# Kernel optimization log

Hardware: AMD Instinct MI355X
Metric: run time of the kernel (lower is better)

Reference implementation:

```python
import jax, jax.numpy as jnp
import numpy as np
from jax import lax

# dims: hidden D, heads H, key head dim DK, value head dim DV (=DK*expand_v), conv size K
B, T, D = 2, 1024, 1024
H, DK, DV, K = 8, 128, 256, 4
EPS = 1e-5  # RMSNorm eps


def short_conv(x, w):
    # depthwise causal conv1d + silu (FLA ShortConvolution, bias=False, activation='silu')
    # x: [B,T,C], w: [C,K]
    Kc = w.shape[-1]
    xp = jnp.pad(x, ((0, 0), (Kc - 1, 0), (0, 0))).transpose(0, 2, 1)  # [B,C,T+K-1]
    y = lax.conv_general_dilated(xp, w[:, None, :], (1,), 'VALID',
                                 feature_group_count=w.shape[0])  # [B,C,T]
    return jax.nn.silu(y.transpose(0, 2, 1))


def l2norm(x):
    return x * lax.rsqrt(jnp.sum(x * x, axis=-1, keepdims=True) + 1e-6)


def gated_delta_rule(q, k, v, g, beta):
    # q,k: [B,T,H,DK]; v: [B,T,H,DV]; g,beta: [B,T,H]
    # recurrence: S_t = exp(g_t)*S_{t-1}; u_t = beta_t*(v_t - k_t^T S_t); S_t += k_t u_t^T; o_t = q_t^T S_t
    scale = q.shape[-1] ** -0.5
    q = l2norm(q) * scale
    k = l2norm(k)
    qT, kT, vT = (a.transpose(1, 0, 2, 3) for a in (q, k, v))  # time-major
    gT, bT = g.transpose(1, 0, 2), beta.transpose(1, 0, 2)
    S0 = jnp.zeros((q.shape[0], q.shape[2], q.shape[3], v.shape[3]), q.dtype)  # [B,H,DK,DV]

    def step(S, inp):
        q_t, k_t, v_t, g_t, b_t = inp
        S = S * jnp.exp(g_t)[..., None, None]
        u = (v_t - jnp.einsum('bhk,bhkv->bhv', k_t, S)) * b_t[..., None]
        S = S + jnp.einsum('bhk,bhv->bhkv', k_t, u)
        o_t = jnp.einsum('bhk,bhkv->bhv', q_t, S)
        return S, o_t

    _, oT = lax.scan(step, S0, (qT, kT, vT, gT, bT))
    return oT.transpose(1, 0, 2, 3)  # [B,T,H,DV]


def setup_inputs() -> dict:
    key = jax.random.key(0)
    ks = jax.random.split(key, 16)
    s = 0.02
    dt = jax.random.uniform(ks[10], (H,), minval=1e-3, maxval=0.1)
    return {
        'x': jax.random.normal(ks[0], (B, T, D), jnp.float32),
        'Wq': jax.random.normal(ks[1], (D, H * DK), jnp.float32) * s,
        'Wk': jax.random.normal(ks[2], (D, H * DK), jnp.float32) * s,
        'Wv': jax.random.normal(ks[3], (D, H * DV), jnp.float32) * s,
        'conv_q': jax.random.normal(ks[4], (H * DK, K), jnp.float32) * 0.2,
        'conv_k': jax.random.normal(ks[5], (H * DK, K), jnp.float32) * 0.2,
        'conv_v': jax.random.normal(ks[6], (H * DV, K), jnp.float32) * 0.2,
        'Wb': jax.random.normal(ks[7], (D, H), jnp.float32) * s,
        'Wa': jax.random.normal(ks[8], (D, H), jnp.float32) * s,
        'A_log': jnp.log(jax.random.uniform(ks[9], (H,), minval=1.0, maxval=16.0)),
        'dt_bias': jnp.log(jnp.expm1(dt)),
        'Wg': jax.random.normal(ks[11], (D, H * DV), jnp.float32) * s,
        'norm_w': jnp.ones((DV,), jnp.float32),
        'Wo': jax.random.normal(ks[12], (H * DV, D), jnp.float32) * s,
    }


def reference(x, Wq, Wk, Wv, conv_q, conv_k, conv_v, Wb, Wa, A_log, dt_bias, Wg, norm_w, Wo):
    Bx, Tx = x.shape[0], x.shape[1]
    q = short_conv(x @ Wq, conv_q).reshape(Bx, Tx, H, DK)
    k = short_conv(x @ Wk, conv_k).reshape(Bx, Tx, H, DK)
    v = short_conv(x @ Wv, conv_v).reshape(Bx, Tx, H, DV)
    beta = jax.nn.sigmoid(x @ Wb)                                  # [B,T,H]
    g = -jnp.exp(A_log) * jax.nn.softplus(x @ Wa + dt_bias)       # [B,T,H], log-decay <= 0
    o = gated_delta_rule(q, k, v, g, beta)                         # [B,T,H,DV]
    # fused gated RMSNorm: rmsnorm(o)*w * silu(g_proj)
    gv = (x @ Wg).reshape(Bx, Tx, H, DV)
    o = o * lax.rsqrt(jnp.mean(o * o, axis=-1, keepdims=True) + EPS) * norm_w
    o = o * jax.nn.silu(gv)
    return o.reshape(Bx, Tx, H * DV) @ Wo
```

## Files before the change

### kernel.cpp

```cpp
#include <hip/hip_runtime.h>
#include <hip/hip_bf16.h>
#include <math.h>

constexpr int Bc = 2, Tc = 1024, Dc = 1024, Hc = 8, DKc = 128, DVc = 256;
constexpr int BT_ROWS = Bc * Tc;
constexpr float QSCALE = 0.08838834764831845f;
constexpr int NCHUNK = 16, CHUNK = 64;

constexpr size_t OF_XB   = 0;
constexpr size_t OF_KBAR = 1048576;
constexpr size_t OF_BTG  = 3145728;
constexpr size_t OF_QPRE = 4194304;
constexpr size_t OF_KPRE = 6291456;
constexpr size_t OF_VPRE = 8388608;
constexpr size_t OF_Q    = 12582912;
constexpr size_t OF_K    = 14680064;
constexpr size_t OF_V    = 4194304;
constexpr size_t OF_G    = 16777216;
constexpr size_t OF_BETA = 16793600;
constexpr size_t OF_O    = 8388608;
constexpr size_t OF_GV   = 12582912;
constexpr size_t OF_OOB  = 4194304;
constexpr size_t OF_WQT  = 12582912;
constexpr size_t OF_WKT  = 13107200;
constexpr size_t OF_WVT  = 13631488;
constexpr size_t OF_WGT  = 1048576;
constexpr size_t OF_WOT  = 2097152;

using short8 = __attribute__((ext_vector_type(8))) short;
using short4v = __attribute__((ext_vector_type(4))) short;
using f32x4  = __attribute__((ext_vector_type(4))) float;

__device__ inline unsigned short f2bf(float f) {
  unsigned int u = __builtin_bit_cast(unsigned int, f);
  u += 0x7FFFu + ((u >> 16) & 1u);
  return (unsigned short)(u >> 16);
}

__device__ inline void gload16(const void* g, void* l) {
  __builtin_amdgcn_global_load_lds(
      (const __attribute__((address_space(1))) unsigned int*)g,
      (__attribute__((address_space(3))) unsigned int*)l, 16, 0, 0);
}

__global__ __launch_bounds__(256) void cvt_bf16(const float* __restrict__ X,
                                                unsigned short* __restrict__ Y) {
  int i = (blockIdx.x * 256 + threadIdx.x) * 4;
  float4 f = *(const float4*)&X[i];
  short4v o = {(short)f2bf(f.x), (short)f2bf(f.y), (short)f2bf(f.z), (short)f2bf(f.w)};
  *(short4v*)&Y[i] = o;
}

__global__ __launch_bounds__(256) void transposeW(const float* __restrict__ W,
                                                  unsigned short* __restrict__ WT,
                                                  int K, int N) {
  __shared__ unsigned short Ls[64 * 66];
  const int n0 = blockIdx.x * 64, k0 = blockIdx.y * 64;
  const int t = threadIdx.x;
  {
    int r = t >> 2, c0 = (t & 3) * 16;
    const float* src = &W[(size_t)(k0 + r) * N + n0 + c0];
#pragma unroll
    for (int m = 0; m < 4; ++m) {
      float4 f = *(const float4*)&src[m * 4];
      unsigned short* p = &Ls[r * 66 + c0 + m * 4];
      p[0] = f2bf(f.x); p[1] = f2bf(f.y); p[2] = f2bf(f.z); p[3] = f2bf(f.w);
    }
  }
  __syncthreads();
  {
    int n = t >> 2, k4 = (t & 3) * 16;
    short8 o0, o1;
#pragma unroll
    for (int j = 0; j < 8; ++j) {
      o0[j] = (short)Ls[(k4 + j) * 66 + n];
      o1[j] = (short)Ls[(k4 + 8 + j) * 66 + n];
    }
    unsigned short* dst = &WT[(size_t)(n0 + n) * K + k0 + k4];
    *(short8*)dst = o0;
    *(short8*)(dst + 8) = o1;
  }
}

template <int TN>
__global__ __launch_bounds__(256) void gemm_nt(const unsigned short* __restrict__ A,
                                               const unsigned short* __restrict__ BT,
                                               float* __restrict__ C,
                                               int M, int N, int K) {
  constexpr int NF = TN / 32;
  __shared__ unsigned short As[128 * 64];
  __shared__ unsigned short Bs[TN * 64];
  const int tid = threadIdx.x, l = tid & 63, w = tid >> 6;
  const int m0 = blockIdx.y * 128, n0 = blockIdx.x * TN;
  const int wm = (w >> 1) * 64, wn = (w & 1) * (TN / 2);
  const int fr = l & 15, hk = l >> 4;
  const int srow = l >> 3, swin = l & 7;
  f32x4 acc[4][NF] = {};

  for (int k0 = 0; k0 < K; k0 += 64) {
#pragma unroll
    for (int i = 0; i < 4; ++i) {
      int ch = i * 4 + w;
      int row = ch * 8 + srow;
      gload16((const char*)(A + (size_t)(m0 + row) * K + k0) + ((swin ^ (row & 7)) * 16),
              (char*)As + ch * 1024);
    }
#pragma unroll
    for (int i = 0; i < TN / 32; ++i) {
      int ch = i * 4 + w;
      int row = ch * 8 + srow;
      gload16((const char*)(BT + (size_t)(n0 + row) * K + k0) + ((swin ^ (row & 7)) * 16),
              (char*)Bs + ch * 1024);
    }
    __syncthreads();
#pragma unroll
    for (int ks = 0; ks < 2; ++ks) {
      short8 a[4], b[NF];
#pragma unroll
      for (int mf = 0; mf < 4; ++mf) {
        int row = wm + mf * 16 + fr;
        a[mf] = *(const short8*)((const char*)As + row * 128 + (((hk + 4 * ks) ^ (row & 7)) * 16));
      }
#pragma unroll
      for (int nf = 0; nf < NF; ++nf) {
        int row = wn + nf * 16 + fr;
        b[nf] = *(const short8*)((const char*)Bs + row * 128 + (((hk + 4 * ks) ^ (row & 7)) * 16));
      }
#pragma unroll
      for (int mf = 0; mf < 4; ++mf)
#pragma unroll
        for (int nf = 0; nf < NF; ++nf)
          acc[mf][nf] = __builtin_amdgcn_mfma_f32_16x16x32_bf16(a[mf], b[nf], acc[mf][nf], 0, 0, 0);
    }
    __syncthreads();
  }
  const int orow = (l >> 4) * 4;
#pragma unroll
  for (int mf = 0; mf < 4; ++mf)
#pragma unroll
    for (int nf = 0; nf < NF; ++nf)
#pragma unroll
      for (int r = 0; r < 4; ++r)
        C[(size_t)(m0 + wm + mf * 16 + orow + r) * N + n0 + wn + nf * 16 + fr] = acc[mf][nf][r];
}

__global__ __launch_bounds__(256) void conv_silu(const float* __restrict__ X,
                                                 const float* __restrict__ W,
                                                 float* __restrict__ Y, int C) {
  int c = blockIdx.x * 256 + threadIdx.x;
  if (c >= C) return;
  int b  = blockIdx.z;
  int t0 = blockIdx.y * 32;
  float4 w = *(const float4*)&W[c * 4];
  const float* xp = X + (size_t)b * Tc * C + c;
  float* yp = Y + (size_t)b * Tc * C + c;
  float x0 = (t0 >= 3) ? xp[(size_t)(t0 - 3) * C] : 0.f;
  float x1 = (t0 >= 2) ? xp[(size_t)(t0 - 2) * C] : 0.f;
  float x2 = (t0 >= 1) ? xp[(size_t)(t0 - 1) * C] : 0.f;
  for (int t = t0; t < t0 + 32; ++t) {
    float x3 = xp[(size_t)t * C];
    float a  = w.x * x0 + w.y * x1 + w.z * x2 + w.w * x3;
    float y  = a / (1.f + __expf(-a));
    yp[(size_t)t * C] = y;
    x0 = x1; x1 = x2; x2 = x3;
  }
}

__global__ __launch_bounds__(256) void beta_g_kernel(const float* __restrict__ X,
                                                     const float* __restrict__ Wb,
                                                     const float* __restrict__ Wa,
                                                     const float* __restrict__ A_log,
                                                     const float* __restrict__ dt_bias,
                                                     float* __restrict__ beta,
                                                     float* __restrict__ glog) {
  int w    = blockIdx.x * 4 + (threadIdx.x >> 6);
  int lane = threadIdx.x & 63;
  int h  = w & 7;
  int bt = w >> 3;
  const float* x = X + (size_t)bt * Dc;
  float sb = 0.f, sa = 0.f;
#pragma unroll
  for (int i = 0; i < 16; ++i) {
    int d = lane + 64 * i;
    float xv = x[d];
    sb = fmaf(xv, Wb[d * 8 + h], sb);
    sa = fmaf(xv, Wa[d * 8 + h], sa);
  }
#pragma unroll
  for (int m = 1; m < 64; m <<= 1) {
    sb += __shfl_xor(sb, m);
    sa += __shfl_xor(sa, m);
  }
  if (lane == 0) {
    beta[w] = 1.f / (1.f + expf(-sb));
    float z  = sa + dt_bias[h];
    float sp = (z > 20.f) ? z : log1pf(expf(z));
    glog[w]  = -expf(A_log[h]) * sp;
  }
}

__global__ __launch_bounds__(256) void l2norm_qk(float* __restrict__ Q, float* __restrict__ K) {
  int w    = blockIdx.x * 4 + (threadIdx.x >> 6);
  int lane = threadIdx.x & 63;
  int h = w & 7;
  size_t bt = (size_t)(w >> 3);
  float* qp = Q + bt * (Hc * DKc) + h * DKc + lane * 2;
  float* kp = K + bt * (Hc * DKc) + h * DKc + lane * 2;
  float2 q2 = *(float2*)qp;
  float2 k2 = *(float2*)kp;
  float sq = q2.x * q2.x + q2.y * q2.y;
  float sk = k2.x * k2.x + k2.y * k2.y;
#pragma unroll
  for (int m = 1; m < 64; m <<= 1) {
    sq += __shfl_xor(sq, m);
    sk += __shfl_xor(sk, m);
  }
  float rq = rsqrtf(sq + 1e-6f) * QSCALE;
  float rk = rsqrtf(sk + 1e-6f);
  q2.x *= rq; q2.y *= rq;
  k2.x *= rk; k2.y *= rk;
  *(float2*)qp = q2;
  *(float2*)kp = k2;
}

__global__ __launch_bounds__(256) void phase1(const float* __restrict__ Q,
                                              const float* __restrict__ K,
                                              float* __restrict__ V,
                                              const float* __restrict__ G,
                                              const float* __restrict__ BETA,
                                              float* __restrict__ Kbar,
                                              float* __restrict__ BTm) {
  constexpr int SK = 68;
  __shared__ float sm[25984];
  float* kcT  = sm;
  float* qcT  = sm + 8704;
  float* vld  = sm;
  float* Amat = sm + 17408;
  float* Mmat = sm + 21568;
  float* cs   = sm + 25728;
  float* bet  = sm + 25856;
  float* wk   = sm + 25920;
  const int tid = threadIdx.x;
  const int c = blockIdx.x, bh = blockIdx.y;
  const int b = bh >> 3, h = bh & 7;
  const int t0 = c * CHUNK;
  const size_t cb = (size_t)bh * NCHUNK + c;

  if (tid < 64) {
    cs[tid]  = G[((size_t)(b * Tc + t0 + tid)) * 8 + h];
    bet[tid] = BETA[((size_t)(b * Tc + t0 + tid)) * 8 + h];
  }
  {
    int r = tid >> 2, dq = (tid & 3) * 32;
    const float4* kg = (const float4*)&K[((size_t)(b * Tc + t0 + r)) * 1024 + h * 128 + dq];
    const float4* qg = (const float4*)&Q[((size_t)(b * Tc + t0 + r)) * 1024 + h * 128 + dq];
#pragma unroll
    for (int m = 0; m < 8; ++m) {
      float4 kv = kg[m], qv = qg[m];
      int d = dq + m * 4;
      kcT[(d + 0) * SK + r] = kv.x; kcT[(d + 1) * SK + r] = kv.y;
      kcT[(d + 2) * SK + r] = kv.z; kcT[(d + 3) * SK + r] = kv.w;
      qcT[(d + 0) * SK + r] = qv.x; qcT[(d + 1) * SK + r] = qv.y;
      qcT[(d + 2) * SK + r] = qv.z; qcT[(d + 3) * SK + r] = qv.w;
    }
  }
  __syncthreads();
  if (tid == 0) {
    float a = 0.f;
    for (int i = 0; i < 64; ++i) { a += cs[i]; cs[i] = a; }
  }
  __syncthreads();
  if (tid < 64) {
    float gv_ = __expf(cs[tid]);
    wk[tid]  = bet[tid] * gv_;
  }
  for (int e = tid; e < 4096; e += 256) {
    int i = e >> 6, s = e & 63;
    float av = 0.f;
    if (s < i) {
      float acc = 0.f;
      for (int d = 0; d < 128; ++d) acc += kcT[d * SK + i] * kcT[d * SK + s];
      av = bet[i] * __expf(cs[i] - cs[s]) * acc;
    }
    Amat[i * 65 + s] = av;
  }
  for (int e = tid; e < 4096; e += 256) {
    int s = e >> 6, i = e & 63;
    float outv = 0.f;
    if (s <= i) {
      float acc = 0.f;
      for (int d = 0; d < 128; ++d) acc += qcT[d * SK + i] * kcT[d * SK + s];
      outv = __expf(cs[i] - cs[s]) * acc;
    }
    BTm[cb * 4096 + (size_t)s * 64 + i] = outv;
  }
  __syncthreads();
  if (tid < 64) {
    int j = tid;
    for (int i = 0; i < 64; ++i) {
      float m = (i == j) ? 1.f : 0.f;
      for (int s = 0; s < i; ++s) m -= Amat[i * 65 + s] * Mmat[s * 65 + j];
      Mmat[i * 65 + j] = m;
    }
  }
  __syncthreads();
  for (int e = tid; e < 2048; e += 256) {
    int i = e & 63, d0 = ((e >> 6) & 31) * 4;
    float a0 = 0, a1 = 0, a2 = 0, a3 = 0;
#pragma unroll 4
    for (int s = 0; s < 64; ++s) {
      float m_ = Mmat[i * 65 + s] * wk[s];
      a0 = fmaf(m_, kcT[(d0 + 0) * SK + s], a0);
      a1 = fmaf(m_, kcT[(d0 + 1) * SK + s], a1);
      a2 = fmaf(m_, kcT[(d0 + 2) * SK + s], a2);
      a3 = fmaf(m_, kcT[(d0 + 3) * SK + s], a3);
    }
    float4 w4 = {a0, a1, a2, a3};
    *(float4*)&Kbar[cb * 8192 + (size_t)i * 128 + d0] = w4;
  }
  __syncthreads();
  {
    int r = tid >> 2, j0 = (tid & 3) * 64;
    const float4* vg = (const float4*)&V[((size_t)(b * Tc + t0 + r)) * 2048 + h * 256 + j0];
#pragma unroll
    for (int m = 0; m < 16; ++m) *(float4*)&vld[r * 256 + j0 + m * 4] = vg[m];
  }
  __syncthreads();
  for (int e = tid; e < 4096; e += 256) {
    int i = e >> 6, j0 = (e & 63) * 4;
    float a0 = 0, a1 = 0, a2 = 0, a3 = 0;
    for (int s = 0; s < 64; ++s) {
      float m_ = Mmat[i * 65 + s] * bet[s];
      float4 vv = *(const float4*)&vld[s * 256 + j0];
      a0 = fmaf(m_, vv.x, a0); a1 = fmaf(m_, vv.y, a1);
      a2 = fmaf(m_, vv.z, a2); a3 = fmaf(m_, vv.w, a3);
    }
    float4 o4 = {a0, a1, a2, a3};
    *(float4*)&V[((size_t)(b * Tc + t0 + i)) * 2048 + h * 256 + j0] = o4;
  }
}

__global__ __launch_bounds__(256) void phase2(const float* __restrict__ KbarG,
                                              const float* __restrict__ BTmG,
                                              const float* __restrict__ GL,
                                              const float* __restrict__ Qp,
                                              const float* __restrict__ Kp,
                                              const float* __restrict__ VBAR,
                                              float* __restrict__ O) {
  __shared__ float S[16 * 132];
  __shared__ float KbL[64 * 128];
  __shared__ float qcL[64 * 128];
  __shared__ float K2L[64 * 128];
  __shared__ float BcL[64 * 64];
  __shared__ float uL[64 * 20];
  __shared__ float csL[64], rsL[64], gamL[64];
  const int tid = threadIdx.x;
  const int l = tid & 63, w = tid >> 6;
  const int jb = blockIdx.y, bh = blockIdx.x;
  const int b = bh >> 3, h = bh & 7;
  const int i = l;
  const int j0 = w * 4;
  const int swzi = (i & 7) << 2;
  const int d0u = (tid & 31) * 4;
  const int jq = tid >> 5;
  const size_t colbase = (size_t)h * 256 + jb * 16;

  for (int e = tid; e < 16 * 132; e += 256) S[e] = 0.f;

  for (int c = 0; c < NCHUNK; ++c) {
    const size_t cb = (size_t)bh * NCHUNK + c;
    const int bT0 = b * Tc + c * CHUNK;
    __syncthreads();
    if (tid < 64) {
      float gi = GL[((size_t)(bT0 + tid)) * 8 + h];
#pragma unroll
      for (int off = 1; off < 64; off <<= 1) {
        float p = __shfl_up(gi, off);
        if (tid >= off) gi += p;
      }
      csL[tid] = gi;
    }
    {
      const char* kbg = (const char*)(KbarG + cb * 8192);
#pragma unroll
      for (int ic = 0; ic < 8; ++ic) {
        int ch = ic * 4 + w;
        int row = 2 * ch + (l >> 5);
        int inrow = (l & 31) * 16;
        int swz = inrow ^ ((row & 7) << 4);
        gload16(kbg + row * 512 + swz, (char*)KbL + ch * 1024);
        gload16((const char*)(Qp + ((size_t)(bT0 + row)) * 1024 + h * 128) + swz,
                (char*)qcL + ch * 1024);
        gload16((const char*)(Kp + ((size_t)(bT0 + row)) * 1024 + h * 128) + inrow,
                (char*)K2L + ch * 1024);
      }
      const char* btg = (const char*)(BTmG + cb * 4096);
#pragma unroll
      for (int ic = 0; ic < 4; ++ic) {
        int ch = ic * 4 + w;
        gload16(btg + ch * 1024 + l * 16, (char*)BcL + ch * 1024);
      }
    }
    __syncthreads();
    if (tid < 64) {
      gamL[tid] = __expf(csL[tid]);
      rsL[tid]  = __expf(csL[63] - csL[tid]);
    }
    float ua[4] = {}, ra[4] = {};
#pragma unroll 4
    for (int d = 0; d < 128; d += 4) {
      int ds = d ^ swzi;
      float4 kb = *(const float4*)&KbL[i * 128 + ds];
      float4 qg = *(const float4*)&qcL[i * 128 + ds];
#pragma unroll
      for (int jj = 0; jj < 4; ++jj) {
        float4 s4 = *(const float4*)&S[(j0 + jj) * 132 + d];
        ua[jj] = fmaf(kb.x, s4.x, fmaf(kb.y, s4.y, fmaf(kb.z, s4.z, fmaf(kb.w, s4.w, ua[jj]))));
        ra[jj] = fmaf(qg.x, s4.x, fmaf(qg.y, s4.y, fmaf(qg.z, s4.z, fmaf(qg.w, s4.w, ra[jj]))));
      }
    }
    float4 vb = *(const float4*)&VBAR[((size_t)(bT0 + i)) * 2048 + colbase + j0];
    float4 uf = {vb.x - ua[0], vb.y - ua[1], vb.z - ua[2], vb.w - ua[3]};
    *(float4*)&uL[i * 20 + j0] = uf;
    __syncthreads();
    float ba[4] = {};
#pragma unroll 4
    for (int s = 0; s < 64; ++s) {
      float bv = BcL[s * 64 + i];
      float4 u4 = *(const float4*)&uL[s * 20 + j0];
      ba[0] = fmaf(bv, u4.x, ba[0]); ba[1] = fmaf(bv, u4.y, ba[1]);
      ba[2] = fmaf(bv, u4.z, ba[2]); ba[3] = fmaf(bv, u4.w, ba[3]);
    }
    float gi = gamL[i];
    float4 o4 = {gi * ra[0] + ba[0], gi * ra[1] + ba[1],
                 gi * ra[2] + ba[2], gi * ra[3] + ba[3]};
    *(float4*)&O[((size_t)(bT0 + i)) * 2048 + colbase + j0] = o4;
    float sa[2][4] = {};
#pragma unroll 4
    for (int s = 0; s < 64; ++s) {
      float4 k2 = *(const float4*)&K2L[s * 128 + d0u];
      float rv = rsL[s];
      float u0 = uL[s * 20 + 2 * jq] * rv;
      float u1 = uL[s * 20 + 2 * jq + 1] * rv;
      sa[0][0] = fmaf(k2.x, u0, sa[0][0]); sa[0][1] = fmaf(k2.y, u0, sa[0][1]);
      sa[0][2] = fmaf(k2.z, u0, sa[0][2]); sa[0][3] = fmaf(k2.w, u0, sa[0][3]);
      sa[1][0] = fmaf(k2.x, u1, sa[1][0]); sa[1][1] = fmaf(k2.y, u1, sa[1][1]);
      sa[1][2] = fmaf(k2.z, u1, sa[1][2]); sa[1][3] = fmaf(k2.w, u1, sa[1][3]);
    }
    float gC = gamL[63];
#pragma unroll
    for (int jj = 0; jj < 2; ++jj) {
      float4 sv = *(const float4*)&S[(2 * jq + jj) * 132 + d0u];
      sv.x = fmaf(gC, sv.x, sa[jj][0]); sv.y = fmaf(gC, sv.y, sa[jj][1]);
      sv.z = fmaf(gC, sv.z, sa[jj][2]); sv.w = fmaf(gC, sv.w, sa[jj][3]);
      *(float4*)&S[(2 * jq + jj) * 132 + d0u] = sv;
    }
  }
}

__global__ __launch_bounds__(256) void gated_rmsnorm(const float* __restrict__ O,
                                                     const float* __restrict__ GV,
                                                     const float* __restrict__ NW,
                                                     unsigned short* __restrict__ OO) {
  int w    = blockIdx.x * 4 + (threadIdx.x >> 6);
  int lane = threadIdx.x & 63;
  size_t base = (size_t)w * DVc;
  float4 o4 = *(const float4*)&O[base + lane * 4];
  float ss = o4.x * o4.x + o4.y * o4.y + o4.z * o4.z + o4.w * o4.w;
#pragma unroll
  for (int m = 1; m < 64; m <<= 1) ss += __shfl_xor(ss, m);
  float r = rsqrtf(ss * (1.f / 256.f) + 1e-5f);
  float4 g4 = *(const float4*)&GV[base + lane * 4];
  float4 w4 = *(const float4*)&NW[lane * 4];
  float4 out;
  out.x = o4.x * r * w4.x * (g4.x / (1.f + __expf(-g4.x)));
  out.y = o4.y * r * w4.y * (g4.y / (1.f + __expf(-g4.y)));
  out.z = o4.z * r * w4.z * (g4.z / (1.f + __expf(-g4.z)));
  out.w = o4.w * r * w4.w * (g4.w / (1.f + __expf(-g4.w)));
  short4v ob = {(short)f2bf(out.x), (short)f2bf(out.y), (short)f2bf(out.z), (short)f2bf(out.w)};
  *(short4v*)&OO[base + lane * 4] = ob;
}

extern "C" void kernel_launch(void* const* d_in, const int* in_sizes, int n_in,
                              void* d_out, int out_size, void* d_ws, size_t ws_size,
                              hipStream_t stream) {
  const float* x       = (const float*)d_in[0];
  const float* Wq      = (const float*)d_in[1];
  const float* Wk      = (const float*)d_in[2];
  const float* Wv      = (const float*)d_in[3];
  const float* conv_q  = (const float*)d_in[4];
  const float* conv_k  = (const float*)d_in[5];
  const float* conv_v  = (const float*)d_in[6];
  const float* Wb      = (const float*)d_in[7];
  const float* Wa      = (const float*)d_in[8];
  const float* A_log   = (const float*)d_in[9];
  const float* dt_bias = (const float*)d_in[10];
  const float* Wg      = (const float*)d_in[11];
  const float* norm_w  = (const float*)d_in[12];
  const float* Wo      = (const float*)d_in[13];
  float* out = (float*)d_out;
  float* ws  = (float*)d_ws;

  unsigned short* xb  = (unsigned short*)(ws + OF_XB);
  unsigned short* WqT = (unsigned short*)(ws + OF_WQT);
  unsigned short* WkT = (unsigned short*)(ws + OF_WKT);
  unsigned short* WvT = (unsigned short*)(ws + OF_WVT);
  unsigned short* WgT = (unsigned short*)(ws + OF_WGT);
  unsigned short* WoT = (unsigned short*)(ws + OF_WOT);
  unsigned short* oob = (unsigned short*)(ws + OF_OOB);
  float* qpre  = ws + OF_QPRE;
  float* kpre  = ws + OF_KPRE;
  float* vpre  = ws + OF_VPRE;
  float* q     = ws + OF_Q;
  float* k     = ws + OF_K;
  float* v     = ws + OF_V;
  float* glog  = ws + OF_G;
  float* beta  = ws + OF_BETA;
  float* Kbar  = ws + OF_KBAR;
  float* BTm   = ws + OF_BTG;
  float* o     = ws + OF_O;
  float* gv    = ws + OF_GV;

  dim3 blk(256);

  cvt_bf16<<<dim3(2048), blk, 0, stream>>>(x, xb);
  transposeW<<<dim3(16, 16), blk, 0, stream>>>(Wq, WqT, 1024, 1024);
  transposeW<<<dim3(16, 16), blk, 0, stream>>>(Wk, WkT, 1024, 1024);
  transposeW<<<dim3(32, 16), blk, 0, stream>>>(Wv, WvT, 1024, 2048);

  gemm_nt<64><<<dim3(16, 16), blk, 0, stream>>>(xb, WqT, qpre, BT_ROWS, 1024, 1024);
  gemm_nt<64><<<dim3(16, 16), blk, 0, stream>>>(xb, WkT, kpre, BT_ROWS, 1024, 1024);
  gemm_nt<128><<<dim3(16, 16), blk, 0, stream>>>(xb, WvT, vpre, BT_ROWS, 2048, 1024);

  beta_g_kernel<<<dim3(BT_ROWS * Hc / 4), blk, 0, stream>>>(x, Wb, Wa, A_log, dt_bias, beta, glog);

  conv_silu<<<dim3(1024 / 256, Tc / 32, Bc), blk, 0, stream>>>(qpre, conv_q, q, 1024);
  conv_silu<<<dim3(1024 / 256, Tc / 32, Bc), blk, 0, stream>>>(kpre, conv_k, k, 1024);
  conv_silu<<<dim3(2048 / 256, Tc / 32, Bc), blk, 0, stream>>>(vpre, conv_v, v, 2048);

  l2norm_qk<<<dim3(BT_ROWS * Hc / 4), blk, 0, stream>>>(q, k);

  phase1<<<dim3(NCHUNK, Bc * Hc), blk, 0, stream>>>(q, k, v, glog, beta, Kbar, BTm);
  phase2<<<dim3(Bc * Hc, 16), blk, 0, stream>>>(Kbar, BTm, glog, q, k, v, o);

  transposeW<<<dim3(32, 16), blk, 0, stream>>>(Wg, WgT, 1024, 2048);
  gemm_nt<128><<<dim3(16, 16), blk, 0, stream>>>(xb, WgT, gv, BT_ROWS, 2048, 1024);

  transposeW<<<dim3(16, 32), blk, 0, stream>>>(Wo, WoT, 2048, 1024);
  gated_rmsnorm<<<dim3(BT_ROWS * Hc / 4), blk, 0, stream>>>(o, gv, norm_w, oob);

  gemm_nt<64><<<dim3(16, 16), blk, 0, stream>>>(oob, WoT, out, BT_ROWS, 1024, 2048);
}
```

Measured before the change: 597.8 us.

## Move chunked delta-rule phase2 matmuls onto bf16 MFMA with bf16 intermediates

Phase1 now writes the per-chunk Kbar, intra-chunk attention matrix, transposed K and Q as bf16 in MFMA-friendly, swizzled layouts. Phase2 replaces its scalar fp32 FMA loops with 16x16x32 bf16 MFMA instructions for the state projections, intra-chunk output and state update. It keeps an fp32 master state plus a bf16 copy refreshed each chunk, and writes the output as bf16. This targets the ALU-bound sequential recurrence and halves intermediate traffic, at the cost of bf16 rounding on the state and the intermediates and an extra barrier per chunk.

```diff
diff --git a/kernel.cpp b/kernel.cpp
--- a/kernel.cpp
+++ b/kernel.cpp
@@ -8,8 +8,9 @@
 constexpr int NCHUNK = 16, CHUNK = 64;
 
 constexpr size_t OF_XB   = 0;
-constexpr size_t OF_KBAR = 1048576;
-constexpr size_t OF_BTG  = 3145728;
+constexpr size_t OF_KB16 = 1048576;
+constexpr size_t OF_K2T  = 2097152;
+constexpr size_t OF_BT16 = 3145728;
 constexpr size_t OF_QPRE = 4194304;
 constexpr size_t OF_KPRE = 6291456;
 constexpr size_t OF_VPRE = 8388608;
@@ -18,7 +19,8 @@
 constexpr size_t OF_V    = 4194304;
 constexpr size_t OF_G    = 16777216;
 constexpr size_t OF_BETA = 16793600;
-constexpr size_t OF_O    = 8388608;
+constexpr size_t OF_OB   = 8388608;
+constexpr size_t OF_QG   = 10485760;
 constexpr size_t OF_GV   = 12582912;
 constexpr size_t OF_OOB  = 4194304;
 constexpr size_t OF_WQT  = 12582912;
@@ -35,6 +37,10 @@
   unsigned int u = __builtin_bit_cast(unsigned int, f);
   u += 0x7FFFu + ((u >> 16) & 1u);
   return (unsigned short)(u >> 16);
+}
+__device__ inline float bf2f(unsigned short u) {
+  unsigned int x = (unsigned int)u << 16;
+  return __builtin_bit_cast(float, x);
 }
 
 __device__ inline void gload16(const void* g, void* l) {
@@ -228,8 +234,10 @@
                                               float* __restrict__ V,
                                               const float* __restrict__ G,
                                               const float* __restrict__ BETA,
-                                              float* __restrict__ Kbar,
-                                              float* __restrict__ BTm) {
+                                              unsigned short* __restrict__ Kb16,
+                                              unsigned short* __restrict__ BT16,
+                                              unsigned short* __restrict__ K2T16,
+                                              unsigned short* __restrict__ QG16) {
   constexpr int SK = 68;
   __shared__ float sm[25984];
   float* kcT  = sm;
@@ -262,6 +270,8 @@
       kcT[(d + 2) * SK + r] = kv.z; kcT[(d + 3) * SK + r] = kv.w;
       qcT[(d + 0) * SK + r] = qv.x; qcT[(d + 1) * SK + r] = qv.y;
       qcT[(d + 2) * SK + r] = qv.z; qcT[(d + 3) * SK + r] = qv.w;
+      short4v qb = {(short)f2bf(qv.x), (short)f2bf(qv.y), (short)f2bf(qv.z), (short)f2bf(qv.w)};
+      *(short4v*)&QG16[cb * 8192 + (size_t)r * 128 + d] = qb;
     }
   }
   __syncthreads();
@@ -285,14 +295,18 @@
     Amat[i * 65 + s] = av;
   }
   for (int e = tid; e < 4096; e += 256) {
-    int s = e >> 6, i = e & 63;
+    int i = e >> 6, s = e & 63;
     float outv = 0.f;
     if (s <= i) {
       float acc = 0.f;
       for (int d = 0; d < 128; ++d) acc += qcT[d * SK + i] * kcT[d * SK + s];
       outv = __expf(cs[i] - cs[s]) * acc;
     }
-    BTm[cb * 4096 + (size_t)s * 64 + i] = outv;
+    BT16[cb * 4096 + (size_t)i * 64 + s] = f2bf(outv);
+  }
+  for (int e = tid; e < 8192; e += 256) {
+    int d = e >> 6, s = e & 63;
+    K2T16[cb * 8192 + (size_t)d * 64 + s] = f2bf(kcT[d * SK + s]);
   }
   __syncthreads();
   if (tid < 64) {
@@ -315,8 +329,8 @@
       a2 = fmaf(m_, kcT[(d0 + 2) * SK + s], a2);
       a3 = fmaf(m_, kcT[(d0 + 3) * SK + s], a3);
     }
-    float4 w4 = {a0, a1, a2, a3};
-    *(float4*)&Kbar[cb * 8192 + (size_t)i * 128 + d0] = w4;
+    short4v w4 = {(short)f2bf(a0), (short)f2bf(a1), (short)f2bf(a2), (short)f2bf(a3)};
+    *(short4v*)&Kb16[cb * 8192 + (size_t)i * 128 + d0] = w4;
   }
   __syncthreads();
   {
@@ -340,37 +354,35 @@
   }
 }
 
-__global__ __launch_bounds__(256) void phase2(const float* __restrict__ KbarG,
-                                              const float* __restrict__ BTmG,
+__global__ __launch_bounds__(256) void phase2(const unsigned short* __restrict__ Kb16,
+                                              const unsigned short* __restrict__ BT16,
+                                              const unsigned short* __restrict__ K2T16,
+                                              const unsigned short* __restrict__ QG16,
                                               const float* __restrict__ GL,
-                                              const float* __restrict__ Qp,
-                                              const float* __restrict__ Kp,
                                               const float* __restrict__ VBAR,
-                                              float* __restrict__ O) {
+                                              unsigned short* __restrict__ Ob) {
   __shared__ float S[16 * 132];
-  __shared__ float KbL[64 * 128];
-  __shared__ float qcL[64 * 128];
-  __shared__ float K2L[64 * 128];
-  __shared__ float BcL[64 * 64];
-  __shared__ float uL[64 * 20];
-  __shared__ float csL[64], rsL[64], gamL[64];
-  const int tid = threadIdx.x;
-  const int l = tid & 63, w = tid >> 6;
-  const int jb = blockIdx.y, bh = blockIdx.x;
+  __shared__ unsigned short Sb[16 * 128];
+  __shared__ unsigned short KbL[64 * 128];
+  __shared__ unsigned short qgL[64 * 128];
+  __shared__ unsigned short K2L[128 * 64];
+  __shared__ unsigned short BtL[64 * 64];
+  __shared__ unsigned short ubT[16 * 64];
+  __shared__ unsigned short rubT[16 * 64];
+  __shared__ float rsL[64], gamL[64];
+  const int tid = threadIdx.x, l = tid & 63, w = tid >> 6;
+  const int bh = blockIdx.x, jb = blockIdx.y;
   const int b = bh >> 3, h = bh & 7;
-  const int i = l;
-  const int j0 = w * 4;
-  const int swzi = (i & 7) << 2;
-  const int d0u = (tid & 31) * 4;
-  const int jq = tid >> 5;
+  const int fr = l & 15, hk = l >> 4;
   const size_t colbase = (size_t)h * 256 + jb * 16;
 
   for (int e = tid; e < 16 * 132; e += 256) S[e] = 0.f;
+  for (int e = tid; e < 2048; e += 256) Sb[e] = 0;
+  __syncthreads();
 
   for (int c = 0; c < NCHUNK; ++c) {
     const size_t cb = (size_t)bh * NCHUNK + c;
     const int bT0 = b * Tc + c * CHUNK;
-    __syncthreads();
     if (tid < 64) {
       float gi = GL[((size_t)(bT0 + tid)) * 8 + h];
 #pragma unroll
@@ -378,106 +390,158 @@
         float p = __shfl_up(gi, off);
         if (tid >= off) gi += p;
       }
-      csL[tid] = gi;
-    }
-    {
-      const char* kbg = (const char*)(KbarG + cb * 8192);
-#pragma unroll
-      for (int ic = 0; ic < 8; ++ic) {
-        int ch = ic * 4 + w;
-        int row = 2 * ch + (l >> 5);
-        int inrow = (l & 31) * 16;
-        int swz = inrow ^ ((row & 7) << 4);
-        gload16(kbg + row * 512 + swz, (char*)KbL + ch * 1024);
-        gload16((const char*)(Qp + ((size_t)(bT0 + row)) * 1024 + h * 128) + swz,
-                (char*)qcL + ch * 1024);
-        gload16((const char*)(Kp + ((size_t)(bT0 + row)) * 1024 + h * 128) + inrow,
-                (char*)K2L + ch * 1024);
-      }
-      const char* btg = (const char*)(BTmG + cb * 4096);
+      float c63 = __shfl(gi, 63);
+      gamL[tid] = __expf(gi);
+      rsL[tid]  = __expf(c63 - gi);
+    }
+    {
+      const char* kb = (const char*)Kb16 + cb * 16384;
+      const char* qg = (const char*)QG16 + cb * 16384;
 #pragma unroll
       for (int ic = 0; ic < 4; ++ic) {
         int ch = ic * 4 + w;
-        gload16(btg + ch * 1024 + l * 16, (char*)BcL + ch * 1024);
+        int row = ch * 4 + (l >> 4);
+        int sw = ((l & 15) * 16) ^ ((row & 7) << 4);
+        gload16(kb + row * 256 + sw, (char*)KbL + ch * 1024);
+        gload16(qg + row * 256 + sw, (char*)qgL + ch * 1024);
+      }
+      const char* kt = (const char*)K2T16 + cb * 16384;
+#pragma unroll
+      for (int ic = 0; ic < 4; ++ic) {
+        int ch = ic * 4 + w;
+        int row = ch * 8 + (l >> 3);
+        int sw = ((l & 7) * 16) ^ ((row & 7) << 4);
+        gload16(kt + row * 128 + sw, (char*)K2L + ch * 1024);
+      }
+      const char* bt = (const char*)BT16 + cb * 8192;
+#pragma unroll
+      for (int ic = 0; ic < 2; ++ic) {
+        int ch = ic * 4 + w;
+        int row = ch * 8 + (l >> 3);
+        int sw = ((l & 7) * 16) ^ ((row & 7) << 4);
+        gload16(bt + row * 128 + sw, (char*)BtL + ch * 1024);
       }
     }
     __syncthreads();
-    if (tid < 64) {
-      gamL[tid] = __expf(csL[tid]);
-      rsL[tid]  = __expf(csL[63] - csL[tid]);
-    }
-    float ua[4] = {}, ra[4] = {};
-#pragma unroll 4
-    for (int d = 0; d < 128; d += 4) {
-      int ds = d ^ swzi;
-      float4 kb = *(const float4*)&KbL[i * 128 + ds];
-      float4 qg = *(const float4*)&qcL[i * 128 + ds];
-#pragma unroll
-      for (int jj = 0; jj < 4; ++jj) {
-        float4 s4 = *(const float4*)&S[(j0 + jj) * 132 + d];
-        ua[jj] = fmaf(kb.x, s4.x, fmaf(kb.y, s4.y, fmaf(kb.z, s4.z, fmaf(kb.w, s4.w, ua[jj]))));
-        ra[jj] = fmaf(qg.x, s4.x, fmaf(qg.y, s4.y, fmaf(qg.z, s4.z, fmaf(qg.w, s4.w, ra[jj]))));
-      }
-    }
-    float4 vb = *(const float4*)&VBAR[((size_t)(bT0 + i)) * 2048 + colbase + j0];
-    float4 uf = {vb.x - ua[0], vb.y - ua[1], vb.z - ua[2], vb.w - ua[3]};
-    *(float4*)&uL[i * 20 + j0] = uf;
+    f32x4 uac = {0.f, 0.f, 0.f, 0.f}, rac = {0.f, 0.f, 0.f, 0.f};
+    {
+      int arow = w * 16 + fr;
+      const char* kbr = (const char*)KbL + arow * 256;
+      const char* qgr = (const char*)qgL + arow * 256;
+      const char* sbr = (const char*)Sb + fr * 256;
+      int asw = (arow & 7) << 4, bsw = (fr & 7) << 4;
+#pragma unroll
+      for (int ks = 0; ks < 4; ++ks) {
+        int ko = hk * 16 + ks * 64;
+        short8 a1 = *(const short8*)(kbr + (ko ^ asw));
+        short8 a2 = *(const short8*)(qgr + (ko ^ asw));
+        short8 bb = *(const short8*)(sbr + (ko ^ bsw));
+        uac = __builtin_amdgcn_mfma_f32_16x16x32_bf16(a1, bb, uac, 0, 0, 0);
+        rac = __builtin_amdgcn_mfma_f32_16x16x32_bf16(a2, bb, rac, 0, 0, 0);
+      }
+    }
+    {
+      int i0 = w * 16 + hk * 4;
+      short4v up, rp;
+#pragma unroll
+      for (int r = 0; r < 4; ++r) {
+        int i = i0 + r;
+        float vb = VBAR[((size_t)(bT0 + i)) * 2048 + colbase + fr];
+        float uv = vb - uac[r];
+        up[r] = (short)f2bf(uv);
+        rp[r] = (short)f2bf(uv * rsL[i]);
+      }
+      int off = fr * 128 + ((i0 * 2) ^ ((fr & 7) << 4));
+      *(short4v*)((char*)ubT + off)  = up;
+      *(short4v*)((char*)rubT + off) = rp;
+    }
     __syncthreads();
-    float ba[4] = {};
-#pragma unroll 4
-    for (int s = 0; s < 64; ++s) {
-      float bv = BcL[s * 64 + i];
-      float4 u4 = *(const float4*)&uL[s * 20 + j0];
-      ba[0] = fmaf(bv, u4.x, ba[0]); ba[1] = fmaf(bv, u4.y, ba[1]);
-      ba[2] = fmaf(bv, u4.z, ba[2]); ba[3] = fmaf(bv, u4.w, ba[3]);
-    }
-    float gi = gamL[i];
-    float4 o4 = {gi * ra[0] + ba[0], gi * ra[1] + ba[1],
-                 gi * ra[2] + ba[2], gi * ra[3] + ba[3]};
-    *(float4*)&O[((size_t)(bT0 + i)) * 2048 + colbase + j0] = o4;
-    float sa[2][4] = {};
-#pragma unroll 4
-    for (int s = 0; s < 64; ++s) {
-      float4 k2 = *(const float4*)&K2L[s * 128 + d0u];
-      float rv = rsL[s];
-      float u0 = uL[s * 20 + 2 * jq] * rv;
-      float u1 = uL[s * 20 + 2 * jq + 1] * rv;
-      sa[0][0] = fmaf(k2.x, u0, sa[0][0]); sa[0][1] = fmaf(k2.y, u0, sa[0][1]);
-      sa[0][2] = fmaf(k2.z, u0, sa[0][2]); sa[0][3] = fmaf(k2.w, u0, sa[0][3]);
-      sa[1][0] = fmaf(k2.x, u1, sa[1][0]); sa[1][1] = fmaf(k2.y, u1, sa[1][1]);
-      sa[1][2] = fmaf(k2.z, u1, sa[1][2]); sa[1][3] = fmaf(k2.w, u1, sa[1][3]);
-    }
-    float gC = gamL[63];
-#pragma unroll
-    for (int jj = 0; jj < 2; ++jj) {
-      float4 sv = *(const float4*)&S[(2 * jq + jj) * 132 + d0u];
-      sv.x = fmaf(gC, sv.x, sa[jj][0]); sv.y = fmaf(gC, sv.y, sa[jj][1]);
-      sv.z = fmaf(gC, sv.z, sa[jj][2]); sv.w = fmaf(gC, sv.w, sa[jj][3]);
-      *(float4*)&S[(2 * jq + jj) * 132 + d0u] = sv;
-    }
-  }
-}
-
-__global__ __launch_bounds__(256) void gated_rmsnorm(const float* __restrict__ O,
+    f32x4 bac = {0.f, 0.f, 0.f, 0.f};
+    {
+      int arow = w * 16 + fr;
+      const char* btr = (const char*)BtL + arow * 128;
+      const char* ubr = (const char*)ubT + fr * 128;
+      int asw = (arow & 7) << 4, bsw = (fr & 7) << 4;
+#pragma unroll
+      for (int ks = 0; ks < 2; ++ks) {
+        int ko = hk * 16 + ks * 64;
+        short8 a = *(const short8*)(btr + (ko ^ asw));
+        short8 bb = *(const short8*)(ubr + (ko ^ bsw));
+        bac = __builtin_amdgcn_mfma_f32_16x16x32_bf16(a, bb, bac, 0, 0, 0);
+      }
+    }
+    {
+      int i0 = w * 16 + hk * 4;
+#pragma unroll
+      for (int r = 0; r < 4; ++r) {
+        int i = i0 + r;
+        float ov = gamL[i] * rac[r] + bac[r];
+        Ob[((size_t)(bT0 + i)) * 2048 + colbase + fr] = f2bf(ov);
+      }
+    }
+    f32x4 sac0 = {0.f, 0.f, 0.f, 0.f}, sac1 = {0.f, 0.f, 0.f, 0.f};
+    {
+      const char* rur = (const char*)rubT + fr * 128;
+      int asw = (fr & 7) << 4;
+      int d0c = (2 * w) * 16 + fr, d1c = (2 * w + 1) * 16 + fr;
+      const char* k0r = (const char*)K2L + d0c * 128;
+      const char* k1r = (const char*)K2L + d1c * 128;
+      int b0sw = (d0c & 7) << 4, b1sw = (d1c & 7) << 4;
+#pragma unroll
+      for (int ks = 0; ks < 2; ++ks) {
+        int ko = hk * 16 + ks * 64;
+        short8 a = *(const short8*)(rur + (ko ^ asw));
+        short8 b0 = *(const short8*)(k0r + (ko ^ b0sw));
+        short8 b1 = *(const short8*)(k1r + (ko ^ b1sw));
+        sac0 = __builtin_amdgcn_mfma_f32_16x16x32_bf16(a, b0, sac0, 0, 0, 0);
+        sac1 = __builtin_amdgcn_mfma_f32_16x16x32_bf16(a, b1, sac1, 0, 0, 0);
+      }
+    }
+    {
+      float gC = gamL[63];
+#pragma unroll
+      for (int r = 0; r < 4; ++r) {
+        int j = hk * 4 + r;
+        int a0 = j * 132 + (2 * w) * 16 + fr;
+        int a1 = j * 132 + (2 * w + 1) * 16 + fr;
+        S[a0] = fmaf(gC, S[a0], sac0[r]);
+        S[a1] = fmaf(gC, S[a1], sac1[r]);
+      }
+    }
+    __syncthreads();
+    {
+      int j = tid >> 4, d0 = (tid & 15) * 8;
+      float4 s0 = *(const float4*)&S[j * 132 + d0];
+      float4 s1 = *(const float4*)&S[j * 132 + d0 + 4];
+      short8 sb8 = {(short)f2bf(s0.x), (short)f2bf(s0.y), (short)f2bf(s0.z), (short)f2bf(s0.w),
+                    (short)f2bf(s1.x), (short)f2bf(s1.y), (short)f2bf(s1.z), (short)f2bf(s1.w)};
+      *(short8*)((char*)Sb + j * 256 + ((d0 * 2) ^ ((j & 7) << 4))) = sb8;
+    }
+    __syncthreads();
+  }
+}
+
+__global__ __launch_bounds__(256) void gated_rmsnorm(const unsigned short* __restrict__ O,
                                                      const float* __restrict__ GV,
                                                      const float* __restrict__ NW,
                                                      unsigned short* __restrict__ OO) {
   int w    = blockIdx.x * 4 + (threadIdx.x >> 6);
   int lane = threadIdx.x & 63;
   size_t base = (size_t)w * DVc;
-  float4 o4 = *(const float4*)&O[base + lane * 4];
-  float ss = o4.x * o4.x + o4.y * o4.y + o4.z * o4.z + o4.w * o4.w;
+  short4v o4v = *(const short4v*)&O[base + lane * 4];
+  float o0 = bf2f((unsigned short)o4v[0]), o1 = bf2f((unsigned short)o4v[1]);
+  float o2 = bf2f((unsigned short)o4v[2]), o3 = bf2f((unsigned short)o4v[3]);
+  float ss = o0 * o0 + o1 * o1 + o2 * o2 + o3 * o3;
 #pragma unroll
   for (int m = 1; m < 64; m <<= 1) ss += __shfl_xor(ss, m);
   float r = rsqrtf(ss * (1.f / 256.f) + 1e-5f);
   float4 g4 = *(const float4*)&GV[base + lane * 4];
   float4 w4 = *(const float4*)&NW[lane * 4];
-  float4 out;
-  out.x = o4.x * r * w4.x * (g4.x / (1.f + __expf(-g4.x)));
-  out.y = o4.y * r * w4.y * (g4.y / (1.f + __expf(-g4.y)));
-  out.z = o4.z * r * w4.z * (g4.z / (1.f + __expf(-g4.z)));
-  out.w = o4.w * r * w4.w * (g4.w / (1.f + __expf(-g4.w)));
-  short4v ob = {(short)f2bf(out.x), (short)f2bf(out.y), (short)f2bf(out.z), (short)f2bf(out.w)};
+  float out0 = o0 * r * w4.x * (g4.x / (1.f + __expf(-g4.x)));
+  float out1 = o1 * r * w4.y * (g4.y / (1.f + __expf(-g4.y)));
+  float out2 = o2 * r * w4.z * (g4.z / (1.f + __expf(-g4.z)));
+  float out3 = o3 * r * w4.w * (g4.w / (1.f + __expf(-g4.w)));
+  short4v ob = {(short)f2bf(out0), (short)f2bf(out1), (short)f2bf(out2), (short)f2bf(out3)};
   *(short4v*)&OO[base + lane * 4] = ob;
 }
 
@@ -501,13 +565,18 @@
   float* out = (float*)d_out;
   float* ws  = (float*)d_ws;
 
-  unsigned short* xb  = (unsigned short*)(ws + OF_XB);
-  unsigned short* WqT = (unsigned short*)(ws + OF_WQT);
-  unsigned short* WkT = (unsigned short*)(ws + OF_WKT);
-  unsigned short* WvT = (unsigned short*)(ws + OF_WVT);
-  unsigned short* WgT = (unsigned short*)(ws + OF_WGT);
-  unsigned short* WoT = (unsigned short*)(ws + OF_WOT);
-  unsigned short* oob = (unsigned short*)(ws + OF_OOB);
+  unsigned short* xb   = (unsigned short*)(ws + OF_XB);
+  unsigned short* Kb16 = (unsigned short*)(ws + OF_KB16);
+  unsigned short* K2T  = (unsigned short*)(ws + OF_K2T);
+  unsigned short* BT16 = (unsigned short*)(ws + OF_BT16);
+  unsigned short* QG16 = (unsigned short*)(ws + OF_QG);
+  unsigned short* ob   = (unsigned short*)(ws + OF_OB);
+  unsigned short* WqT  = (unsigned short*)(ws + OF_WQT);
+  unsigned short* WkT  = (unsigned short*)(ws + OF_WKT);
+  unsigned short* WvT  = (unsigned short*)(ws + OF_WVT);
+  unsigned short* WgT  = (unsigned short*)(ws + OF_WGT);
+  unsigned short* WoT  = (unsigned short*)(ws + OF_WOT);
+  unsigned short* oob  = (unsigned short*)(ws + OF_OOB);
   float* qpre  = ws + OF_QPRE;
   float* kpre  = ws + OF_KPRE;
   float* vpre  = ws + OF_VPRE;
@@ -516,9 +585,6 @@
   float* v     = ws + OF_V;
   float* glog  = ws + OF_G;
   float* beta  = ws + OF_BETA;
-  float* Kbar  = ws + OF_KBAR;
-  float* BTm   = ws + OF_BTG;
-  float* o     = ws + OF_O;
   float* gv    = ws + OF_GV;
 
   dim3 blk(256);
@@ -540,14 +606,14 @@
 
   l2norm_qk<<<dim3(BT_ROWS * Hc / 4), blk, 0, stream>>>(q, k);
 
-  phase1<<<dim3(NCHUNK, Bc * Hc), blk, 0, stream>>>(q, k, v, glog, beta, Kbar, BTm);
-  phase2<<<dim3(Bc * Hc, 16), blk, 0, stream>>>(Kbar, BTm, glog, q, k, v, o);
+  phase1<<<dim3(NCHUNK, Bc * Hc), blk, 0, stream>>>(q, k, v, glog, beta, Kb16, BT16, K2T, QG16);
+  phase2<<<dim3(Bc * Hc, 16), blk, 0, stream>>>(Kb16, BT16, K2T, QG16, glog, v, ob);
 
   transposeW<<<dim3(32, 16), blk, 0, stream>>>(Wg, WgT, 1024, 2048);
   gemm_nt<128><<<dim3(16, 16), blk, 0, stream>>>(xb, WgT, gv, BT_ROWS, 2048, 1024);
 
   transposeW<<<dim3(16, 32), blk, 0, stream>>>(Wo, WoT, 2048, 1024);
-  gated_rmsnorm<<<dim3(BT_ROWS * Hc / 4), blk, 0, stream>>>(o, gv, norm_w, oob);
+  gated_rmsnorm<<<dim3(BT_ROWS * Hc / 4), blk, 0, stream>>>(ob, gv, norm_w, oob);
 
   gemm_nt<64><<<dim3(16, 16), blk, 0, stream>>>(oob, WoT, out, BT_ROWS, 1024, 2048);
 }
```

Result: faster. 489.1 us (-18.2%).
